# Performance work log

Measured on AMD Instinct MI355X. Metric: run time of the kernel, lower is better.

Reference implementation:

```python
import jax, jax.numpy as jnp
import numpy as np

# dims
D_MODEL = 256; D_STATE = 16; D_CONV = 4; EXPAND = 2
D_INNER = D_MODEL * EXPAND            # 512
DT_RANK = 16                          # ceil(256/16)
B_SZ = 16; C_IN = 64; T_LR = 2560; R = 2; C_OUT = 64


def _p(key, shape, scale=0.02):
    return jax.random.normal(key, shape, jnp.float32) * scale


def setup_inputs() -> dict:
    key = jax.random.key(0)
    ks = iter(jax.random.split(key, 48))
    inp = {}
    inp['x'] = jax.random.normal(next(ks), (B_SZ, C_IN, T_LR), jnp.float32)
    # encoder: Conv1d(64->128,k3,p1) ; Conv1d(128->256,k3,p1)
    inp['enc_w1'] = _p(next(ks), (128, C_IN, 3)); inp['enc_b1'] = jnp.zeros((128,), jnp.float32)
    inp['enc_w2'] = _p(next(ks), (256, 128, 3)); inp['enc_b2'] = jnp.zeros((256,), jnp.float32)
    # BidirectionalMamba norms
    inp['norm1_w'] = jnp.ones((D_MODEL,), jnp.float32)
    inp['norm2_w'] = jnp.ones((D_MODEL,), jnp.float32)
    # one forward ('f') and one backward ('b') Mamba v1 block
    for p in ('f', 'b'):
        inp[p + '_inW'] = _p(next(ks), (2 * D_INNER, D_MODEL))
        inp[p + '_convW'] = _p(next(ks), (D_INNER, D_CONV), 0.2)
        inp[p + '_convb'] = jnp.zeros((D_INNER,), jnp.float32)
        inp[p + '_xW'] = _p(next(ks), (DT_RANK + 2 * D_STATE, D_INNER))
        inp[p + '_dtW'] = _p(next(ks), (D_INNER, DT_RANK), 0.1)
        inp[p + '_dtb'] = -4.0 + 2.0 * jax.random.uniform(next(ks), (D_INNER,), jnp.float32)
        inp[p + '_Alog'] = jnp.log(jnp.tile(jnp.arange(1, D_STATE + 1, dtype=jnp.float32), (D_INNER, 1)))
        inp[p + '_D'] = jnp.ones((D_INNER,), jnp.float32)
        inp[p + '_outW'] = _p(next(ks), (D_MODEL, D_INNER))
    # post-bottleneck: Conv1d(512->256,k3,p1) + BatchNorm1d(256) (eval)
    inp['convd_w'] = _p(next(ks), (256, 512, 3)); inp['convd_b'] = jnp.zeros((256,), jnp.float32)
    inp['bn_g'] = jnp.ones((256,), jnp.float32); inp['bn_b'] = jnp.zeros((256,), jnp.float32)
    inp['bn_mean'] = jnp.zeros((256,), jnp.float32); inp['bn_var'] = jnp.ones((256,), jnp.float32)
    # SubPixel1D: Conv1d(256 -> target_channels*r, k3, p1), r=2
    inp['sp_w'] = _p(next(ks), (C_OUT * R, 256, 3)); inp['sp_b'] = jnp.zeros((C_OUT * R,), jnp.float32)
    return inp


def silu(x):
    return x * jax.nn.sigmoid(x)


def conv1d(x, w, b):  # x: (B,C,L), w: (O,I,K), 'same' padding
    k = w.shape[-1]
    y = jax.lax.conv_general_dilated(x, w, (1,), [(k // 2, k // 2)],
                                     dimension_numbers=('NCH', 'OIH', 'NCH'))
    return y + b[None, :, None]


def rmsnorm(x, w, eps=1e-6):
    return x * jax.lax.rsqrt(jnp.mean(x * x, -1, keepdims=True) + eps) * w


def mamba(x, inW, convW, convb, xW, dtW, dtb, Alog, Dp, outW):
    # x: (B, L, D_MODEL) -> (B, L, D_MODEL); Mamba v1 selective scan.
    Bn = x.shape[0]
    xz = x @ inW.T                               # (B,L,2*di)
    xc, z = jnp.split(xz, 2, axis=-1)            # (B,L,di) each
    # causal depthwise conv over time
    xt = jnp.transpose(xc, (0, 2, 1))            # (B,di,L)
    xt = jax.lax.conv_general_dilated(xt, convW[:, None, :], (1,), [(D_CONV - 1, 0)],
                                      dimension_numbers=('NCH', 'OIH', 'NCH'),
                                      feature_group_count=D_INNER)
    xc = silu(jnp.transpose(xt + convb[None, :, None], (0, 2, 1)))  # (B,L,di)
    dbc = xc @ xW.T                              # (B,L,dt_rank+2N)
    dt = jax.nn.softplus(dbc[..., :DT_RANK] @ dtW.T + dtb)          # (B,L,di)
    Bc = dbc[..., DT_RANK:DT_RANK + D_STATE]     # (B,L,N)
    Cc = dbc[..., DT_RANK + D_STATE:]            # (B,L,N)
    A = -jnp.exp(Alog)                           # (di,N)

    def step(h, inp):
        dt_t, B_t, C_t, x_t = inp                # (B,di),(B,N),(B,N),(B,di)
        dA = jnp.exp(dt_t[..., None] * A)        # (B,di,N)
        h = dA * h + (dt_t * x_t)[..., None] * B_t[:, None, :]
        y = jnp.einsum('bdn,bn->bd', h, C_t)
        return h, y

    xs = (jnp.transpose(dt, (1, 0, 2)), jnp.transpose(Bc, (1, 0, 2)),
          jnp.transpose(Cc, (1, 0, 2)), jnp.transpose(xc, (1, 0, 2)))
    h0 = jnp.zeros((Bn, D_INNER, D_STATE), x.dtype)
    _, ys = jax.lax.scan(step, h0, xs)           # ys: (L,B,di)
    y = jnp.transpose(ys, (1, 0, 2)) + xc * Dp
    return (y * silu(z)) @ outW.T


def reference(x, enc_w1, enc_b1, enc_w2, enc_b2, norm1_w, norm2_w,
              f_inW, f_convW, f_convb, f_xW, f_dtW, f_dtb, f_Alog, f_D, f_outW,
              b_inW, b_convW, b_convb, b_xW, b_dtW, b_dtb, b_Alog, b_D, b_outW,
              convd_w, convd_b, bn_g, bn_b, bn_mean, bn_var, sp_w, sp_b):
    # encoder (dropout = identity in eval)
    e = silu(conv1d(x, enc_w1, enc_b1))
    e = silu(conv1d(e, enc_w2, enc_b2))          # (B,256,T)
    t = jnp.transpose(e, (0, 2, 1))              # (B,T,256)
    # Bi-Mamba bottleneck layer
    xn = rmsnorm(t, norm1_w)
    mo_f = mamba(xn, f_inW, f_convW, f_convb, f_xW, f_dtW, f_dtb, f_Alog, f_D, f_outW) + xn
    xb = xn[:, ::-1, :]
    mo_b = mamba(xb, b_inW, b_convW, b_convb, b_xW, b_dtW, b_dtb, b_Alog, b_D, b_outW) + xb
    mo_b = mo_b[:, ::-1, :]
    combined = rmsnorm(mo_f + mo_b, norm2_w)
    m = jnp.concatenate([combined, t], axis=-1)  # (B,T,512)
    m = jnp.transpose(m, (0, 2, 1))              # (B,512,T)
    # conv_d + BatchNorm1d (eval) + SiLU
    d = conv1d(m, convd_w, convd_b)
    d = (d - bn_mean[None, :, None]) * jax.lax.rsqrt(bn_var + 1e-5)[None, :, None] \
        * bn_g[None, :, None] + bn_b[None, :, None]
    d = silu(d)
    # SubPixel1D upsample x2
    s = conv1d(d, sp_w, sp_b)                    # (B, C_OUT*R, T)
    Bn, C, T = s.shape
    s = s.reshape(Bn, C // R, R, T).transpose(0, 1, 3, 2).reshape(Bn, C // R, T * R)
    return s                                      # (B, 64, 5120)
```

## Files before the change

### kernel.cpp

```cpp
#include <hip/hip_runtime.h>
#include <hip/hip_bf16.h>
#include <math.h>

#define B_SZ 16
#define T_LR 2560
#define BT (B_SZ * T_LR)
#define DM 256
#define DI 512
#define DS 16
#define DTR 16
#define CH 128
#define CH_LOG2 7
#define CLEN (T_LR / CH)

typedef __attribute__((ext_vector_type(8))) short bf16x8;
typedef __attribute__((ext_vector_type(4))) float f32x4;

__device__ __forceinline__ float silu_f(float x) {
    return x / (1.f + __expf(-x));
}
__device__ __forceinline__ unsigned short f2bf(float v) {
    __hip_bfloat16 h = __float2bfloat16(v);
    return *(unsigned short*)&h;
}
__device__ __forceinline__ float bf2f(unsigned short u) {
    union { unsigned int i; float f; } c;
    c.i = (unsigned int)u << 16;
    return c.f;
}
__device__ __forceinline__ int seqrev(int r) {
    int s = r / T_LR, t = r % T_LR;
    return s * T_LR + (T_LR - 1 - t);
}
__device__ __forceinline__ float softplus_f(float x) {
    return (x > 20.f) ? x : __logf(1.f + __expf(x));
}

__global__ __launch_bounds__(256) void k_prep(
    const float* __restrict__ enc_w1, const float* __restrict__ enc_w2,
    const float* __restrict__ convd_w, const float* __restrict__ sp_w,
    const float* __restrict__ convd_b, const float* __restrict__ bn_g,
    const float* __restrict__ bn_b, const float* __restrict__ bn_mean,
    const float* __restrict__ bn_var,
    const float* __restrict__ inW0, const float* __restrict__ inW1,
    const float* __restrict__ outW0, const float* __restrict__ outW1,
    const float* __restrict__ xW0, const float* __restrict__ xW1,
    const float* __restrict__ Alog0, const float* __restrict__ Alog1,
    const float* __restrict__ x,
    unsigned short* __restrict__ W1r, unsigned short* __restrict__ W2r,
    unsigned short* __restrict__ Wdr, unsigned short* __restrict__ Wspr,
    float* __restrict__ alpha, float* __restrict__ beta,
    unsigned short* __restrict__ inW_bf2, unsigned short* __restrict__ outW_bf2,
    unsigned short* __restrict__ xW_bc2, float* __restrict__ Aflag,
    unsigned short* __restrict__ xt)
{
    __shared__ float ts[32][33];
    __shared__ int s_ok;
    int blk = blockIdx.x;
    int tid = threadIdx.x;
    if (blk < 32) {
        int i = blk * 256 + tid;
        int n = i / 64, ci = i % 64;
        #pragma unroll
        for (int k = 0; k < 3; k++)
            W1r[((size_t)k * 128 + n) * 64 + ci] = f2bf(enc_w1[((size_t)n * 64 + ci) * 3 + k]);
    } else if (blk < 160) {
        int i = (blk - 32) * 256 + tid;
        int n = i / 128, ci = i % 128;
        #pragma unroll
        for (int k = 0; k < 3; k++)
            W2r[((size_t)k * 256 + n) * 128 + ci] = f2bf(enc_w2[((size_t)n * 128 + ci) * 3 + k]);
    } else if (blk < 672) {
        int i = (blk - 160) * 256 + tid;
        int n = i / 512, ci = i % 512;
        #pragma unroll
        for (int k = 0; k < 3; k++)
            Wdr[((size_t)k * 256 + n) * 512 + ci] = f2bf(convd_w[((size_t)n * 512 + ci) * 3 + k]);
    } else if (blk < 800) {
        int i = (blk - 672) * 256 + tid;
        int n = i / 256, ci = i % 256;
        #pragma unroll
        for (int k = 0; k < 3; k++)
            Wspr[((size_t)k * 128 + n) * 256 + ci] = f2bf(sp_w[((size_t)n * 256 + ci) * 3 + k]);
    } else if (blk < 801) {
        int c = tid;
        float a = bn_g[c] * rsqrtf(bn_var[c] + 1e-5f);
        alpha[c] = a;
        beta[c] = (convd_b[c] - bn_mean[c]) * a + bn_b[c];
    } else if (blk < 1825) {
        int i = (blk - 801) * 256 + tid;
        inW_bf2[i] = f2bf(inW0[i]);
        inW_bf2[262144 + i] = f2bf(inW1[i]);
    } else if (blk < 2337) {
        int i = (blk - 1825) * 256 + tid;
        outW_bf2[i] = f2bf(outW0[i]);
        outW_bf2[131072 + i] = f2bf(outW1[i]);
    } else if (blk < 2433) {
        int i = (blk - 2337) * 256 + tid;
        xW_bc2[i] = f2bf(xW0[i]);
        xW_bc2[24576 + i] = f2bf(xW1[i]);
    } else if (blk < 2434) {
        if (tid == 0) s_ok = 1;
        __syncthreads();
        int ok = 1;
        for (int i = tid; i < DI * DS; i += 256) {
            int d = i >> 4, n = i & 15;
            float a0f = __expf(Alog0[d * DS]);
            float anf = __expf(Alog0[d * DS + n]);
            if (fabsf(anf - (float)(n + 1) * a0f) > 1e-3f * (float)(n + 1)) ok = 0;
            float a0b = __expf(Alog1[d * DS]);
            float anb = __expf(Alog1[d * DS + n]);
            if (fabsf(anb - (float)(n + 1) * a0b) > 1e-3f * (float)(n + 1)) ok = 0;
        }
        if (!ok) atomicAnd(&s_ok, 0);
        __syncthreads();
        if (tid == 0) Aflag[0] = s_ok ? 1.f : 0.f;
    } else {
        int idx = blk - 2434;
        int t0 = (idx % 80) * 32;
        int c0 = ((idx / 80) & 1) * 32;
        int b = idx / 160;
        int tx = tid & 31, ty = tid >> 5;
        #pragma unroll
        for (int j = 0; j < 4; j++) {
            int c = c0 + ty + j * 8;
            ts[ty + j * 8][tx] = x[((size_t)b * 64 + c) * T_LR + t0 + tx];
        }
        __syncthreads();
        #pragma unroll
        for (int j = 0; j < 4; j++) {
            int t = t0 + ty + j * 8;
            xt[((size_t)b * T_LR + t) * 64 + c0 + tx] = f2bf(ts[tx][ty + j * 8]);
        }
    }
}

__global__ __launch_bounds__(256, 3) void k_conv3_bf(const unsigned short* __restrict__ A1, int K1,
                                                  const unsigned short* __restrict__ A2, int K2,
                                                  const unsigned short* __restrict__ W,
                                                  const float* __restrict__ alpha,
                                                  const float* __restrict__ beta,
                                                  float* __restrict__ outf,
                                                  unsigned short* __restrict__ outb,
                                                  int N, int dosilu, int pixsh) {
    int Kt = K1 + K2;
    __shared__ unsigned short As[2][130][40];
    int tid = threadIdx.x;
    int wave = tid >> 6, lane = tid & 63;
    int wm = (wave >> 1) * 64, wn = (wave & 1) * 64;
    int m0 = blockIdx.x * 128, n0 = blockIdx.y * 128;
    int b = m0 / T_LR, t0 = m0 % T_LR;
    int q = lane >> 4, ml = lane & 15;
    const unsigned short* wbase = W + (size_t)(n0 + wn + ml) * Kt + q * 8;
    size_t tapstride = (size_t)N * Kt;
    size_t nistride  = (size_t)16 * Kt;
    f32x4 acc[4][4] = {};
    int cq = tid & 3;
    int r0 = tid >> 2;
    int r1 = r0 + 64;
    int r2 = r0 + 128;
    bool has2 = (tid < 8);
    int ta0 = t0 - 1 + r0, ta1 = t0 - 1 + r1, ta2 = t0 - 1 + r2;
    bool va0 = (ta0 >= 0) && (ta0 < T_LR);
    bool va1 = (ta1 < T_LR);
    bool va2 = has2 && (ta2 < T_LR);
    uint4 v0, v1, v2;
    #define LOADA(vv, valid, t, col) { vv = make_uint4(0u,0u,0u,0u); if (valid) { \
        const unsigned short* src = ((col) < K1) \
            ? A1 + (size_t)(b * T_LR + (t)) * K1 + (col) \
            : A2 + (size_t)(b * T_LR + (t)) * K2 + ((col) - K1); \
        vv = *(const uint4*)src; } }
    LOADA(v0, va0, ta0, cq * 8);
    LOADA(v1, va1, ta1, cq * 8);
    LOADA(v2, va2, ta2, cq * 8);
    *(uint4*)&As[0][r0][cq * 8] = v0;
    *(uint4*)&As[0][r1][cq * 8] = v1;
    if (has2) *(uint4*)&As[0][r2][cq * 8] = v2;
    int nk = Kt >> 5;
    for (int kk = 0; kk < nk; kk++) {
        __syncthreads();
        int cur = kk & 1;
        int k0 = kk << 5;
        if (kk + 1 < nk) {
            int col = k0 + 32 + cq * 8;
            LOADA(v0, va0, ta0, col);
            LOADA(v1, va1, ta1, col);
            LOADA(v2, va2, ta2, col);
        }
        #pragma unroll
        for (int tap = 0; tap < 3; tap++) {
            bf16x8 bfr[4];
            #pragma unroll
            for (int ni = 0; ni < 4; ni++)
                bfr[ni] = *(const bf16x8*)(wbase + tap * tapstride + ni * nistride + k0);
            #pragma unroll
            for (int mi = 0; mi < 4; mi++) {
                bf16x8 af = *(const bf16x8*)&As[cur][wm + mi * 16 + ml + tap][q * 8];
                #pragma unroll
                for (int ni = 0; ni < 4; ni++)
                    acc[mi][ni] = __builtin_amdgcn_mfma_f32_16x16x32_bf16(af, bfr[ni], acc[mi][ni], 0, 0, 0);
            }
        }
        if (kk + 1 < nk) {
            *(uint4*)&As[cur ^ 1][r0][cq * 8] = v0;
            *(uint4*)&As[cur ^ 1][r1][cq * 8] = v1;
            if (has2) *(uint4*)&As[cur ^ 1][r2][cq * 8] = v2;
        }
    }
    #undef LOADA
    #pragma unroll
    for (int mi = 0; mi < 4; mi++) {
        #pragma unroll
        for (int r = 0; r < 4; r++) {
            int mr = m0 + wm + mi * 16 + q * 4 + r;
            int t = mr - b * T_LR;
            #pragma unroll
            for (int ni = 0; ni < 4; ni++) {
                int col = n0 + wn + ni * 16 + ml;
                float a = alpha ? alpha[col] : 1.f;
                float v = acc[mi][ni][r] * a + beta[col];
                if (dosilu) v = silu_f(v);
                if (pixsh) {
                    int c2 = col >> 1, rr = col & 1;
                    outf[(((size_t)b * 64 + c2) * T_LR + t) * 2 + rr] = v;
                } else {
                    size_t o = (size_t)mr * N + col;
                    if (outf) outf[o] = v;
                    if (outb) outb[o] = f2bf(v);
                }
            }
        }
    }
}

__global__ __launch_bounds__(256) void k_inproj_conv(const unsigned short* __restrict__ xn,
                                                     const unsigned short* __restrict__ inW,
                                                     const float* __restrict__ cw,
                                                     const float* __restrict__ cb,
                                                     unsigned short* __restrict__ xcs,
                                                     int arev) {
    __shared__ unsigned short As[128][40];
    __shared__ unsigned short Bs[128][40];
    __shared__ unsigned short Ct[131][136];
    int tid = threadIdx.x;
    int wave = tid >> 6, lane = tid & 63;
    int wm = (wave >> 1) * 64, wn = (wave & 1) * 64;
    int m0 = blockIdx.x * 128, n0 = blockIdx.y * 128;
    int b = m0 / T_LR, t0 = m0 % T_LR;
    int sc = tid & 3, sr = tid >> 2;
    int ar0 = m0 + sr, ar1 = m0 + sr + 64;
    if (arev) { ar0 = seqrev(ar0); ar1 = seqrev(ar1); }
    const unsigned short* ap0 = xn + (size_t)ar0 * DM + sc * 8;
    const unsigned short* ap1 = xn + (size_t)ar1 * DM + sc * 8;
    const unsigned short* bp0 = inW + (size_t)(n0 + sr) * DM + sc * 8;
    const unsigned short* bp1 = inW + (size_t)(n0 + sr + 64) * DM + sc * 8;
    f32x4 acc[4][4] = {};
    int q = lane >> 4, ml = lane & 15;
    for (int k0 = 0; k0 < DM; k0 += 32) {
        uint4 a0 = *(const uint4*)(ap0 + k0);
        uint4 a1 = *(const uint4*)(ap1 + k0);
        uint4 b0 = *(const uint4*)(bp0 + k0);
        uint4 b1 = *(const uint4*)(bp1 + k0);
        __syncthreads();
        *(uint4*)&As[sr][sc * 8]      = a0;
        *(uint4*)&As[sr + 64][sc * 8] = a1;
        *(uint4*)&Bs[sr][sc * 8]      = b0;
        *(uint4*)&Bs[sr + 64][sc * 8] = b1;
        __syncthreads();
        bf16x8 af[4], bfr[4];
        #pragma unroll
        for (int mi = 0; mi < 4; mi++)
            af[mi] = *(const bf16x8*)&As[wm + mi * 16 + ml][q * 8];
        #pragma unroll
        for (int ni = 0; ni < 4; ni++)
            bfr[ni] = *(const bf16x8*)&Bs[wn + ni * 16 + ml][q * 8];
        #pragma unroll
        for (int mi = 0; mi < 4; mi++)
            #pragma unroll
            for (int ni = 0; ni < 4; ni++)
                acc[mi][ni] = __builtin_amdgcn_mfma_f32_16x16x32_bf16(af[mi], bfr[ni], acc[mi][ni], 0, 0, 0);
    }
    #pragma unroll
    for (int mi = 0; mi < 4; mi++)
        #pragma unroll
        for (int r = 0; r < 4; r++)
            #pragma unroll
            for (int ni = 0; ni < 4; ni++)
                Ct[3 + wm + mi * 16 + q * 4 + r][wn + ni * 16 + ml] = f2bf(acc[mi][ni][r]);
    for (int i = tid; i < 384; i += 256) {
        int hr = i >> 7, c = i & 127;
        int tr = t0 - 3 + hr;
        float v = 0.f;
        if (tr >= 0) {
            int src = b * T_LR + (arev ? (T_LR - 1 - tr) : tr);
            const unsigned short* xr = xn + (size_t)src * DM;
            const unsigned short* wr = inW + (size_t)(n0 + c) * DM;
            for (int k = 0; k < DM; k += 8) {
                uint4 xa = *(const uint4*)(xr + k);
                uint4 wa = *(const uint4*)(wr + k);
                const unsigned short* xs = (const unsigned short*)&xa;
                const unsigned short* wsp = (const unsigned short*)&wa;
                #pragma unroll
                for (int j = 0; j < 8; j++) v += bf2f(xs[j]) * bf2f(wsp[j]);
            }
        }
        Ct[hr][c] = f2bf(v);
    }
    __syncthreads();
    int col = tid & 127;
    int d = n0 + col;
    float w0 = cw[d * 4 + 0], w1 = cw[d * 4 + 1], w2 = cw[d * 4 + 2], w3 = cw[d * 4 + 3];
    float bi = cb[d];
    int rbase = tid >> 7;
    for (int j = 0; j < 64; j++) {
        int row = rbase + 2 * j;
        float v = bi + bf2f(Ct[row][col]) * w0 + bf2f(Ct[row + 1][col]) * w1
                     + bf2f(Ct[row + 2][col]) * w2 + bf2f(Ct[row + 3][col]) * w3;
        xcs[(size_t)(m0 + row) * DI + d] = f2bf(silu_f(v));
    }
}

__global__ __launch_bounds__(256) void k_rmsnorm(const float* __restrict__ in1,
                                                 const float* __restrict__ w,
                                                 float* __restrict__ out,
                                                 unsigned short* __restrict__ out_bf,
                                                 int ntok) {
    int tok = (blockIdx.x * 256 + threadIdx.x) >> 6;
    int lane = threadIdx.x & 63;
    if (tok >= ntok) return;
    float4 v = ((const float4*)(in1 + (size_t)tok * DM))[lane];
    float ss = v.x * v.x + v.y * v.y + v.z * v.z + v.w * v.w;
    #pragma unroll
    for (int off = 32; off > 0; off >>= 1) ss += __shfl_xor(ss, off);
    float sc = rsqrtf(ss * (1.f / 256.f) + 1e-6f);
    float4 wv = ((const float4*)w)[lane];
    float4 o;
    o.x = v.x * sc * wv.x; o.y = v.y * sc * wv.y;
    o.z = v.z * sc * wv.z; o.w = v.w * sc * wv.w;
    if (out) ((float4*)(out + (size_t)tok * DM))[lane] = o;
    if (out_bf) {
        ushort4 ob;
        ob.x = f2bf(o.x); ob.y = f2bf(o.y); ob.z = f2bf(o.z); ob.w = f2bf(o.w);
        ((ushort4*)(out_bf + (size_t)tok * DM))[lane] = ob;
    }
}

__global__ __launch_bounds__(256) void k_gemm_bf(const unsigned short* __restrict__ A, int lda,
                                                 const unsigned short* __restrict__ Bw,
                                                 float* Cf, unsigned short* Cb, int ldc,
                                                 const float* __restrict__ res,
                                                 const float* __restrict__ bias,
                                                 const unsigned short* __restrict__ gate,
                                                 int K, int Nout, int act,
                                                 int arev, int crev, int accum) {
    __shared__ unsigned short As[128][40];
    __shared__ unsigned short Bs[128][40];
    int tid = threadIdx.x;
    int wave = tid >> 6, lane = tid & 63;
    int wm = (wave >> 1) * 64, wn = (wave & 1) * 64;
    int m0 = blockIdx.x * 128, n0 = blockIdx.y * 128;
    int sc = tid & 3, sr = tid >> 2;
    int ar0 = m0 + sr, ar1 = m0 + sr + 64;
    if (arev) { ar0 = seqrev(ar0); ar1 = seqrev(ar1); }
    const unsigned short* ap0 = A + (size_t)ar0 * lda + sc * 8;
    const unsigned short* ap1 = A + (size_t)ar1 * lda + sc * 8;
    bool bv0 = (n0 + sr) < Nout;
    bool bv1 = (n0 + sr + 64) < Nout;
    const unsigned short* bp0 = Bw + (size_t)(n0 + sr) * K + sc * 8;
    const unsigned short* bp1 = Bw + (size_t)(n0 + sr + 64) * K + sc * 8;
    f32x4 acc[4][4] = {};
    int q = lane >> 4, ml = lane & 15;
    for (int k0 = 0; k0 < K; k0 += 32) {
        uint4 a0 = *(const uint4*)(ap0 + k0);
        uint4 a1 = *(const uint4*)(ap1 + k0);
        uint4 b0 = make_uint4(0u, 0u, 0u, 0u), b1 = make_uint4(0u, 0u, 0u, 0u);
        if (bv0) b0 = *(const uint4*)(bp0 + k0);
        if (bv1) b1 = *(const uint4*)(bp1 + k0);
        __syncthreads();
        *(uint4*)&As[sr][sc * 8]      = a0;
        *(uint4*)&As[sr + 64][sc * 8] = a1;
        *(uint4*)&Bs[sr][sc * 8]      = b0;
        *(uint4*)&Bs[sr + 64][sc * 8] = b1;
        __syncthreads();
        bf16x8 af[4], bfr[4];
        #pragma unroll
        for (int mi = 0; mi < 4; mi++)
            af[mi] = *(const bf16x8*)&As[wm + mi * 16 + ml][q * 8];
        #pragma unroll
        for (int ni = 0; ni < 4; ni++)
            bfr[ni] = *(const bf16x8*)&Bs[wn + ni * 16 + ml][q * 8];
        #pragma unroll
        for (int mi = 0; mi < 4; mi++)
            #pragma unroll
            for (int ni = 0; ni < 4; ni++)
                acc[mi][ni] = __builtin_amdgcn_mfma_f32_16x16x32_bf16(af[mi], bfr[ni], acc[mi][ni], 0, 0, 0);
    }
    #pragma unroll
    for (int mi = 0; mi < 4; mi++) {
        #pragma unroll
        for (int r = 0; r < 4; r++) {
            int mr = m0 + wm + mi * 16 + q * 4 + r;
            int orow = crev ? seqrev(mr) : mr;
            #pragma unroll
            for (int ni = 0; ni < 4; ni++) {
                int col = n0 + wn + ni * 16 + ml;
                if (col < Nout) {
                    float v = acc[mi][ni][r];
                    if (bias) v += bias[col];
                    if (act == 2) v = softplus_f(v);
                    if (gate) v = silu_f(v) * bf2f(gate[(size_t)mr * ldc + col]);
                    if (res) v += res[(size_t)orow * ldc + col];
                    if (accum) v += Cf[(size_t)orow * ldc + col];
                    if (Cf) Cf[(size_t)orow * ldc + col] = v;
                    if (Cb) Cb[(size_t)orow * ldc + col] = f2bf(v);
                }
            }
        }
    }
}

__global__ __launch_bounds__(256) void k_gemm_bf_cb(const unsigned short* __restrict__ A, int lda,
                                                    const unsigned short* __restrict__ Bw,
                                                    unsigned short* __restrict__ Cb, int ldc,
                                                    const float* __restrict__ bias,
                                                    const unsigned short* __restrict__ gate,
                                                    int K, int act, int arev) {
    __shared__ __align__(16) unsigned short smem[2 * 128 * 40];
    unsigned short (*As)[40] = (unsigned short(*)[40])smem;
    unsigned short (*Bs)[40] = (unsigned short(*)[40])(smem + 128 * 40);
    float* sC = (float*)smem;
    int tid = threadIdx.x;
    int wave = tid >> 6, lane = tid & 63;
    int wm = (wave >> 1) * 64, wn = (wave & 1) * 64;
    int m0 = blockIdx.x * 128, n0 = blockIdx.y * 128;
    int sc = tid & 3, sr = tid >> 2;
    int ar0 = m0 + sr, ar1 = m0 + sr + 64;
    if (arev) { ar0 = seqrev(ar0); ar1 = seqrev(ar1); }
    const unsigned short* ap0 = A + (size_t)ar0 * lda + sc * 8;
    const unsigned short* ap1 = A + (size_t)ar1 * lda + sc * 8;
    const unsigned short* bp0 = Bw + (size_t)(n0 + sr) * K + sc * 8;
    const unsigned short* bp1 = Bw + (size_t)(n0 + sr + 64) * K + sc * 8;
    f32x4 acc[4][4] = {};
    int q = lane >> 4, ml = lane & 15;
    for (int k0 = 0; k0 < K; k0 += 32) {
        uint4 a0 = *(const uint4*)(ap0 + k0);
        uint4 a1 = *(const uint4*)(ap1 + k0);
        uint4 b0 = *(const uint4*)(bp0 + k0);
        uint4 b1 = *(const uint4*)(bp1 + k0);
        __syncthreads();
        *(uint4*)&As[sr][sc * 8]      = a0;
        *(uint4*)&As[sr + 64][sc * 8] = a1;
        *(uint4*)&Bs[sr][sc * 8]      = b0;
        *(uint4*)&Bs[sr + 64][sc * 8] = b1;
        __syncthreads();
        bf16x8 af[4], bfr[4];
        #pragma unroll
        for (int mi = 0; mi < 4; mi++)
            af[mi] = *(const bf16x8*)&As[wm + mi * 16 + ml][q * 8];
        #pragma unroll
        for (int ni = 0; ni < 4; ni++)
            bfr[ni] = *(const bf16x8*)&Bs[wn + ni * 16 + ml][q * 8];
        #pragma unroll
        for (int mi = 0; mi < 4; mi++)
            #pragma unroll
            for (int ni = 0; ni < 4; ni++)
                acc[mi][ni] = __builtin_amdgcn_mfma_f32_16x16x32_bf16(af[mi], bfr[ni], acc[mi][ni], 0, 0, 0);
    }
    #pragma unroll
    for (int p = 0; p < 4; p++) {
        __syncthreads();
        if ((wave >> 1) == (p >> 1)) {
            int mib = (p & 1) * 2;
            #pragma unroll
            for (int m2 = 0; m2 < 2; m2++) {
                int mi = mib + m2;
                int rl = mi * 16 + q * 4 - (p & 1) * 32;
                #pragma unroll
                for (int r = 0; r < 4; r++)
                    #pragma unroll
                    for (int ni = 0; ni < 4; ni++)
                        sC[(rl + r) * 140 + wn + ni * 16 + ml] = acc[mi][ni][r];
            }
        }
        __syncthreads();
        #pragma unroll
        for (int gi = 0; gi < 2; gi++) {
            int g = tid + gi * 256;
            int row = g >> 4;
            int colg = (g & 15) * 8;
            int grow = m0 + p * 32 + row;
            const float* src = sC + row * 140 + colg;
            float4 v0 = *(const float4*)src;
            float4 v1 = *(const float4*)(src + 4);
            float vv[8] = {v0.x, v0.y, v0.z, v0.w, v1.x, v1.y, v1.z, v1.w};
            unsigned short gu[8];
            if (gate)
                *(uint4*)gu = *(const uint4*)(gate + (size_t)grow * ldc + n0 + colg);
            unsigned short o[8];
            #pragma unroll
            for (int jj = 0; jj < 8; jj++) {
                float v = vv[jj];
                if (bias) v += bias[n0 + colg + jj];
                if (act == 2) v = softplus_f(v);
                if (gate) v = silu_f(v) * bf2f(gu[jj]);
                o[jj] = f2bf(v);
            }
            *(uint4*)(Cb + (size_t)grow * ldc + n0 + colg) = *(uint4*)o;
        }
    }
}

__global__ __launch_bounds__(256) void k_scan_p1(const unsigned short* __restrict__ x,
                                                 const float* __restrict__ db,
                                                 const float* __restrict__ dtW,
                                                 const float* __restrict__ dtb,
                                                 const float* __restrict__ Alog,
                                                 const float* __restrict__ Aflag,
                                                 float* __restrict__ hS,
                                                 float* __restrict__ csum) {
    __shared__ float dbs[CLEN * 48];
    int tid = threadIdx.x;
    int gid = blockIdx.x * 256 + tid;
    int d = gid & (DI - 1);
    int bcix = gid >> 9;
    int c = bcix & (CH - 1);
    int bl = bcix >> CH_LOG2;
    int tbase = c * CLEN;
    const float* dbp = db + ((size_t)bl * T_LR + tbase) * 48;
    if (tid < 240) *(float4*)&dbs[tid * 4] = *(const float4*)(dbp + tid * 4);
    bool fast = (Aflag[0] != 0.f);
    float A0 = -__expf(Alog[d * DS]);
    float Av[DS], h[DS];
    #pragma unroll
    for (int n = 0; n < DS; n++) h[n] = 0.f;
    if (!fast) {
        #pragma unroll
        for (int n = 0; n < DS; n++) Av[n] = -__expf(Alog[d * DS + n]);
    }
    const float4* wp = (const float4*)(dtW + d * 16);
    float4 w0 = wp[0], w1 = wp[1], w2 = wp[2], w3 = wp[3];
    float bias = dtb[d];
    const unsigned short* xp = x + ((size_t)bl * T_LR + tbase) * DI + d;
    float S = 0.f;
    __syncthreads();
    for (int t = 0; t < CLEN; t++) {
        const float* bc = dbs + t * 48;
        float dl = bias
            + bc[0] * w0.x + bc[1] * w0.y + bc[2] * w0.z + bc[3] * w0.w
            + bc[4] * w1.x + bc[5] * w1.y + bc[6] * w1.z + bc[7] * w1.w
            + bc[8] * w2.x + bc[9] * w2.y + bc[10] * w2.z + bc[11] * w2.w
            + bc[12] * w3.x + bc[13] * w3.y + bc[14] * w3.z + bc[15] * w3.w;
        float dtv = softplus_f(dl);
        float xv  = bf2f(xp[(size_t)t * DI]);
        float dtx = dtv * xv;
        S += dtv;
        if (fast) {
            float e1 = __expf(dtv * A0);
            float e = e1;
            #pragma unroll
            for (int n = 0; n < DS; n++) {
                h[n] = e * h[n] + dtx * bc[16 + n];
                e *= e1;
            }
        } else {
            #pragma unroll
            for (int n = 0; n < DS; n++)
                h[n] = __expf(dtv * Av[n]) * h[n] + dtx * bc[16 + n];
        }
    }
    float* hp = hS + (size_t)gid * DS;
    #pragma unroll
    for (int n = 0; n < DS; n++) hp[n] = h[n];
    csum[gid] = S;
}

__global__ __launch_bounds__(256) void k_scan_p2(float* __restrict__ hS,
                                                 const float* __restrict__ csum,
                                                 const float* __restrict__ Alog) {
    int gid = blockIdx.x * 256 + threadIdx.x;
    int n = gid & (DS - 1);
    int d = (gid >> 4) & (DI - 1);
    int bl = gid >> 13;
    float An = -__expf(Alog[d * DS + n]);
    float hs = 0.f;
    for (int c = 0; c < CH; c++) {
        size_t base = ((size_t)(bl * CH + c) * DI + d);
        float he = hS[base * DS + n];
        float S  = csum[base];
        hS[base * DS + n] = hs;
        hs = __expf(An * S) * hs + he;
    }
}

__global__ __launch_bounds__(256) void k_scan_p3(unsigned short* __restrict__ x,
                                                 const float* __restrict__ db,
                                                 const float* __restrict__ dtW,
                                                 const float* __restrict__ dtb,
                                                 const float* __restrict__ Alog,
                                                 const float* __restrict__ Aflag,
                                                 const float* __restrict__ Dp,
                                                 const float* __restrict__ hS) {
    __shared__ float dbs[CLEN * 48];
    int tid = threadIdx.x;
    int gid = blockIdx.x * 256 + tid;
    int d = gid & (DI - 1);
    int bcix = gid >> 9;
    int c = bcix & (CH - 1);
    int bl = bcix >> CH_LOG2;
    int tbase = c * CLEN;
    const float* dbp = db + ((size_t)bl * T_LR + tbase) * 48;
    if (tid < 240) *(float4*)&dbs[tid * 4] = *(const float4*)(dbp + tid * 4);
    bool fast = (Aflag[0] != 0.f);
    float A0 = -__expf(Alog[d * DS]);
    float Av[DS], h[DS];
    const float* hp = hS + (size_t)gid * DS;
    #pragma unroll
    for (int n = 0; n < DS; n++) h[n] = hp[n];
    if (!fast) {
        #pragma unroll
        for (int n = 0; n < DS; n++) Av[n] = -__expf(Alog[d * DS + n]);
    }
    const float4* wp = (const float4*)(dtW + d * 16);
    float4 w0 = wp[0], w1 = wp[1], w2 = wp[2], w3 = wp[3];
    float bias = dtb[d];
    float Dd = Dp[d];
    unsigned short* xp = x + ((size_t)bl * T_LR + tbase) * DI + d;
    __syncthreads();
    for (int t = 0; t < CLEN; t++) {
        const float* bc = dbs + t * 48;
        float dl = bias
            + bc[0] * w0.x + bc[1] * w0.y + bc[2] * w0.z + bc[3] * w0.w
            + bc[4] * w1.x + bc[5] * w1.y + bc[6] * w1.z + bc[7] * w1.w
            + bc[8] * w2.x + bc[9] * w2.y + bc[10] * w2.z + bc[11] * w2.w
            + bc[12] * w3.x + bc[13] * w3.y + bc[14] * w3.z + bc[15] * w3.w;
        float dtv = softplus_f(dl);
        float xv  = bf2f(xp[(size_t)t * DI]);
        float dtx = dtv * xv;
        float acc = 0.f;
        if (fast) {
            float e1 = __expf(dtv * A0);
            float e = e1;
            #pragma unroll
            for (int n = 0; n < DS; n++) {
                h[n] = e * h[n] + dtx * bc[16 + n];
                acc += h[n] * bc[32 + n];
                e *= e1;
            }
        } else {
            #pragma unroll
            for (int n = 0; n < DS; n++) {
                h[n] = __expf(dtv * Av[n]) * h[n] + dtx * bc[16 + n];
                acc += h[n] * bc[32 + n];
            }
        }
        xp[(size_t)t * DI] = f2bf(acc + xv * Dd);
    }
}

extern "C" void kernel_launch(void* const* d_in, const int* in_sizes, int n_in,
                              void* d_out, int out_size, void* d_ws, size_t ws_size,
                              hipStream_t stream) {
    const float* x       = (const float*)d_in[0];
    const float* enc_w1  = (const float*)d_in[1];
    const float* enc_b1  = (const float*)d_in[2];
    const float* enc_w2  = (const float*)d_in[3];
    const float* enc_b2  = (const float*)d_in[4];
    const float* norm1_w = (const float*)d_in[5];
    const float* norm2_w = (const float*)d_in[6];
    const float* convd_w = (const float*)d_in[25];
    const float* convd_b = (const float*)d_in[26];
    const float* bn_g    = (const float*)d_in[27];
    const float* bn_b    = (const float*)d_in[28];
    const float* bn_mean = (const float*)d_in[29];
    const float* bn_var  = (const float*)d_in[30];
    const float* sp_w    = (const float*)d_in[31];
    const float* sp_b    = (const float*)d_in[32];
    float* out = (float*)d_out;

    const float* inW0   = (const float*)d_in[7];
    const float* xW0    = (const float*)d_in[10];
    const float* outW0  = (const float*)d_in[15];
    const float* inW1   = (const float*)d_in[16];
    const float* xW1    = (const float*)d_in[19];
    const float* outW1  = (const float*)d_in[24];
    const float* Alog0  = (const float*)d_in[13];
    const float* Alog1  = (const float*)d_in[22];

    float* ws = (float*)d_ws;
    size_t availf = ws_size / sizeof(float);
    size_t o = 0;
    float* t_buf  = ws + o; o += (size_t)BT * DM;
    float* xn_buf = ws + o; o += (size_t)BT * DM;
    float* mo     = ws + o; o += (size_t)BT * DM;
    unsigned short* xn_bf = (unsigned short*)(ws + o); o += (size_t)BT * DM / 2;
    unsigned short* tb_bf = (unsigned short*)(ws + o); o += (size_t)BT * DM / 2;
    unsigned short* inW_bf2  = (unsigned short*)(ws + o); o += (size_t)1024 * DM;
    unsigned short* outW_bf2 = (unsigned short*)(ws + o); o += (size_t)DM * DI;
    unsigned short* xW_bc2   = (unsigned short*)(ws + o); o += (size_t)48 * DI;
    unsigned short* W1r  = (unsigned short*)(ws + o); o += (3 * 128 * 64) / 2;
    unsigned short* W2r  = (unsigned short*)(ws + o); o += (3 * 256 * 128) / 2;
    unsigned short* Wdr  = (unsigned short*)(ws + o); o += (3 * 256 * 512) / 2;
    unsigned short* Wspr = (unsigned short*)(ws + o); o += (3 * 128 * 256) / 2;
    float* alpha_d = ws + o; o += 256;
    float* beta_d  = ws + o; o += 256;
    float* Aflag_d = ws + o; o += 4;
    size_t persist = o;
    float* scratch = ws + persist;
    size_t scratch_avail = (availf > persist) ? (availf - persist) : 0;
    size_t per_b = (size_t)T_LR * DI / 2 * 2 + (size_t)T_LR * 48
                 + (size_t)CH * DI * (DS + 1);
    int Bc = 16;
    while (Bc > 1 && (size_t)Bc * per_b > scratch_avail) Bc >>= 1;

    unsigned short* xt  = (unsigned short*)mo;
    unsigned short* e1t = (unsigned short*)(mo + (size_t)BT * 64 / 2);
    unsigned short* comb_bf = (unsigned short*)xn_buf;
    unsigned short* d_bf = (unsigned short*)mo;

    k_prep<<<4994, 256, 0, stream>>>(enc_w1, enc_w2, convd_w, sp_w,
                                     convd_b, bn_g, bn_b, bn_mean, bn_var,
                                     inW0, inW1, outW0, outW1, xW0, xW1,
                                     Alog0, Alog1,
                                     x, W1r, W2r, Wdr, Wspr, alpha_d, beta_d,
                                     inW_bf2, outW_bf2, xW_bc2, Aflag_d, xt);

    k_conv3_bf<<<dim3(BT / 128, 1), 256, 0, stream>>>(xt, 64, nullptr, 0, W1r,
                                                      nullptr, enc_b1, nullptr, e1t, 128, 1, 0);
    k_conv3_bf<<<dim3(BT / 128, 2), 256, 0, stream>>>(e1t, 128, nullptr, 0, W2r,
                                                      nullptr, enc_b2, t_buf, tb_bf, 256, 1, 0);
    k_rmsnorm<<<BT / 4, 256, 0, stream>>>(t_buf, norm1_w, xn_buf, xn_bf, BT);

    for (int dir = 0; dir < 2; dir++) {
        const float* convW = (const float*)d_in[8 + 9 * dir];
        const float* convb = (const float*)d_in[9 + 9 * dir];
        const float* dtW   = (const float*)d_in[11 + 9 * dir];
        const float* dtb   = (const float*)d_in[12 + 9 * dir];
        const float* Alog  = (const float*)d_in[13 + 9 * dir];
        const float* Dp    = (const float*)d_in[14 + 9 * dir];
        const unsigned short* inW_d  = inW_bf2 + (size_t)dir * 1024 * DM;
        const unsigned short* outW_d = outW_bf2 + (size_t)dir * DM * DI;
        const unsigned short* xWbc_d = xW_bc2 + (size_t)dir * 48 * DI;
        int rev = dir;
        for (int b0 = 0; b0 < B_SZ; b0 += Bc) {
            int Tc = Bc * T_LR;
            unsigned short* xcs = (unsigned short*)scratch;
            unsigned short* ygb = xcs + (size_t)Tc * DI;
            float* db   = (float*)(ygb + (size_t)Tc * DI);
            float* hS   = db + (size_t)Tc * 48;
            float* csum = hS + (size_t)Bc * CH * DI * DS;
            const float*          xnC  = xn_buf + (size_t)b0 * T_LR * DM;
            const unsigned short* xnbC = xn_bf  + (size_t)b0 * T_LR * DM;
            float*                moC  = mo     + (size_t)b0 * T_LR * DM;
            k_inproj_conv<<<dim3(Tc / 128, DI / 128), 256, 0, stream>>>(
                xnbC, inW_d, convW, convb, xcs, rev);
            k_gemm_bf<<<dim3(Tc / 128, 1), 256, 0, stream>>>(
                xcs, DI, xWbc_d, db, nullptr, 48, nullptr, nullptr, nullptr,
                DI, 48, 0, 0, 0, 0);
            k_scan_p1<<<(Bc * CH * DI) / 256, 256, 0, stream>>>(xcs, db, dtW, dtb, Alog, Aflag_d, hS, csum);
            k_scan_p2<<<(Bc * DI * DS) / 256, 256, 0, stream>>>(hS, csum, Alog);
            k_scan_p3<<<(Bc * CH * DI) / 256, 256, 0, stream>>>(xcs, db, dtW, dtb, Alog, Aflag_d, Dp, hS);
            k_gemm_bf_cb<<<dim3(Tc / 128, DI / 128), 256, 0, stream>>>(
                xnbC, DM, inW_d + (size_t)DI * DM, ygb, DI, nullptr, xcs, DM, 0, rev);
            k_gemm_bf<<<dim3(Tc / 128, DM / 128), 256, 0, stream>>>(
                ygb, DI, outW_d, moC, nullptr, DM, xnC, nullptr, nullptr,
                DI, DM, 0, 0, rev, dir);
        }
    }

    k_rmsnorm<<<BT / 4, 256, 0, stream>>>(mo, norm2_w, nullptr, comb_bf, BT);
    k_conv3_bf<<<dim3(BT / 128, 2), 256, 0, stream>>>(comb_bf, 256, tb_bf, 256, Wdr,
                                                      alpha_d, beta_d, nullptr, d_bf, 256, 1, 0);
    k_conv3_bf<<<dim3(BT / 128, 1), 256, 0, stream>>>(d_bf, 256, nullptr, 0, Wspr,
                                                      nullptr, sp_b, out, nullptr, 128, 0, 1);
}
```

Measured before the change: 1.318 ms.

## Batch forward and backward Mamba directions into shared launches via blockIdx.z

```diff
diff --git a/kernel.cpp b/kernel.cpp
--- a/kernel.cpp
+++ b/kernel.cpp
@@ -234,14 +234,22 @@
 }
 
 __global__ __launch_bounds__(256) void k_inproj_conv(const unsigned short* __restrict__ xn,
-                                                     const unsigned short* __restrict__ inW,
-                                                     const float* __restrict__ cw,
-                                                     const float* __restrict__ cb,
+                                                     const unsigned short* __restrict__ inW2,
+                                                     const float* __restrict__ cw0,
+                                                     const float* __restrict__ cw1,
+                                                     const float* __restrict__ cb0,
+                                                     const float* __restrict__ cb1,
                                                      unsigned short* __restrict__ xcs,
-                                                     int arev) {
+                                                     long long dsXcs) {
     __shared__ unsigned short As[128][40];
     __shared__ unsigned short Bs[128][40];
     __shared__ unsigned short Ct[131][136];
+    int dir = blockIdx.z;
+    int arev = dir;
+    const unsigned short* inW = inW2 + (size_t)dir * 1024 * DM;
+    const float* cw = dir ? cw1 : cw0;
+    const float* cb = dir ? cb1 : cb0;
+    xcs += (size_t)dir * dsXcs;
     int tid = threadIdx.x;
     int wave = tid >> 6, lane = tid & 63;
     int wm = (wave >> 1) * 64, wn = (wave & 1) * 64;
@@ -321,6 +329,7 @@
 }
 
 __global__ __launch_bounds__(256) void k_rmsnorm(const float* __restrict__ in1,
+                                                 const float* __restrict__ in2,
                                                  const float* __restrict__ w,
                                                  float* __restrict__ out,
                                                  unsigned short* __restrict__ out_bf,
@@ -329,6 +338,10 @@
     int lane = threadIdx.x & 63;
     if (tok >= ntok) return;
     float4 v = ((const float4*)(in1 + (size_t)tok * DM))[lane];
+    if (in2) {
+        float4 u = ((const float4*)(in2 + (size_t)tok * DM))[lane];
+        v.x += u.x; v.y += u.y; v.z += u.z; v.w += u.w;
+    }
     float ss = v.x * v.x + v.y * v.y + v.z * v.z + v.w * v.w;
     #pragma unroll
     for (int off = 32; off > 0; off >>= 1) ss += __shfl_xor(ss, off);
@@ -345,25 +358,25 @@
     }
 }
 
-__global__ __launch_bounds__(256) void k_gemm_bf(const unsigned short* __restrict__ A, int lda,
-                                                 const unsigned short* __restrict__ Bw,
-                                                 float* Cf, unsigned short* Cb, int ldc,
+__global__ __launch_bounds__(256) void k_gemm_bf(const unsigned short* __restrict__ A, int lda, long long dsA,
+                                                 const unsigned short* __restrict__ Bw, long long dsB,
+                                                 float* Cf, long long dsCf, int ldc,
                                                  const float* __restrict__ res,
-                                                 const float* __restrict__ bias,
-                                                 const unsigned short* __restrict__ gate,
-                                                 int K, int Nout, int act,
-                                                 int arev, int crev, int accum) {
+                                                 int K, int Nout, int crevmode) {
     __shared__ unsigned short As[128][40];
     __shared__ unsigned short Bs[128][40];
+    int dir = blockIdx.z;
+    A += (long long)dir * dsA;
+    Bw += (long long)dir * dsB;
+    Cf += (long long)dir * dsCf;
+    int crev = (crevmode == 2) ? dir : crevmode;
     int tid = threadIdx.x;
     int wave = tid >> 6, lane = tid & 63;
     int wm = (wave >> 1) * 64, wn = (wave & 1) * 64;
     int m0 = blockIdx.x * 128, n0 = blockIdx.y * 128;
     int sc = tid & 3, sr = tid >> 2;
-    int ar0 = m0 + sr, ar1 = m0 + sr + 64;
-    if (arev) { ar0 = seqrev(ar0); ar1 = seqrev(ar1); }
-    const unsigned short* ap0 = A + (size_t)ar0 * lda + sc * 8;
-    const unsigned short* ap1 = A + (size_t)ar1 * lda + sc * 8;
+    const unsigned short* ap0 = A + (size_t)(m0 + sr) * lda + sc * 8;
+    const unsigned short* ap1 = A + (size_t)(m0 + sr + 64) * lda + sc * 8;
     bool bv0 = (n0 + sr) < Nout;
     bool bv1 = (n0 + sr + 64) < Nout;
     const unsigned short* bp0 = Bw + (size_t)(n0 + sr) * K + sc * 8;
@@ -406,13 +419,8 @@
                 int col = n0 + wn + ni * 16 + ml;
                 if (col < Nout) {
                     float v = acc[mi][ni][r];
-                    if (bias) v += bias[col];
-                    if (act == 2) v = softplus_f(v);
-                    if (gate) v = silu_f(v) * bf2f(gate[(size_t)mr * ldc + col]);
                     if (res) v += res[(size_t)orow * ldc + col];
-                    if (accum) v += Cf[(size_t)orow * ldc + col];
-                    if (Cf) Cf[(size_t)orow * ldc + col] = v;
-                    if (Cb) Cb[(size_t)orow * ldc + col] = f2bf(v);
+                    Cf[(size_t)orow * ldc + col] = v;
                 }
             }
         }
@@ -420,15 +428,19 @@
 }
 
 __global__ __launch_bounds__(256) void k_gemm_bf_cb(const unsigned short* __restrict__ A, int lda,
-                                                    const unsigned short* __restrict__ Bw,
-                                                    unsigned short* __restrict__ Cb, int ldc,
-                                                    const float* __restrict__ bias,
-                                                    const unsigned short* __restrict__ gate,
-                                                    int K, int act, int arev) {
+                                                    const unsigned short* __restrict__ Bw, long long dsB,
+                                                    unsigned short* __restrict__ Cb, int ldc, long long dsCb,
+                                                    const unsigned short* __restrict__ gate, long long dsGate,
+                                                    int K) {
     __shared__ __align__(16) unsigned short smem[2 * 128 * 40];
     unsigned short (*As)[40] = (unsigned short(*)[40])smem;
     unsigned short (*Bs)[40] = (unsigned short(*)[40])(smem + 128 * 40);
     float* sC = (float*)smem;
+    int dir = blockIdx.z;
+    int arev = dir;
+    Bw += (long long)dir * dsB;
+    Cb += (long long)dir * dsCb;
+    gate += (long long)dir * dsGate;
     int tid = threadIdx.x;
     int wave = tid >> 6, lane = tid & 63;
     int wm = (wave >> 1) * 64, wn = (wave & 1) * 64;
@@ -494,15 +506,12 @@
             float4 v1 = *(const float4*)(src + 4);
             float vv[8] = {v0.x, v0.y, v0.z, v0.w, v1.x, v1.y, v1.z, v1.w};
             unsigned short gu[8];
-            if (gate)
-                *(uint4*)gu = *(const uint4*)(gate + (size_t)grow * ldc + n0 + colg);
+            *(uint4*)gu = *(const uint4*)(gate + (size_t)grow * ldc + n0 + colg);
             unsigned short o[8];
             #pragma unroll
             for (int jj = 0; jj < 8; jj++) {
                 float v = vv[jj];
-                if (bias) v += bias[n0 + colg + jj];
-                if (act == 2) v = softplus_f(v);
-                if (gate) v = silu_f(v) * bf2f(gu[jj]);
+                v = silu_f(v) * bf2f(gu[jj]);
                 o[jj] = f2bf(v);
             }
             *(uint4*)(Cb + (size_t)grow * ldc + n0 + colg) = *(uint4*)o;
@@ -512,12 +521,12 @@
 
 __global__ __launch_bounds__(256) void k_scan_p1(const unsigned short* __restrict__ x,
                                                  const float* __restrict__ db,
-                                                 const float* __restrict__ dtW,
-                                                 const float* __restrict__ dtb,
-                                                 const float* __restrict__ Alog,
+                                                 const float* __restrict__ dtW0, const float* __restrict__ dtW1,
+                                                 const float* __restrict__ dtb0, const float* __restrict__ dtb1,
+                                                 const float* __restrict__ Alog0, const float* __restrict__ Alog1,
                                                  const float* __restrict__ Aflag,
                                                  float* __restrict__ hS,
-                                                 float* __restrict__ csum) {
+                                                 float* __restrict__ csum, int Bc) {
     __shared__ float dbs[CLEN * 48];
     int tid = threadIdx.x;
     int gid = blockIdx.x * 256 + tid;
@@ -525,6 +534,10 @@
     int bcix = gid >> 9;
     int c = bcix & (CH - 1);
     int bl = bcix >> CH_LOG2;
+    int dir = (bl >= Bc) ? 1 : 0;
+    const float* dtW  = dir ? dtW1  : dtW0;
+    const float* dtb  = dir ? dtb1  : dtb0;
+    const float* Alog = dir ? Alog1 : Alog0;
     int tbase = c * CLEN;
     const float* dbp = db + ((size_t)bl * T_LR + tbase) * 48;
     if (tid < 240) *(float4*)&dbs[tid * 4] = *(const float4*)(dbp + tid * 4);
@@ -576,11 +589,13 @@
 
 __global__ __launch_bounds__(256) void k_scan_p2(float* __restrict__ hS,
                                                  const float* __restrict__ csum,
-                                                 const float* __restrict__ Alog) {
+                                                 const float* __restrict__ Alog0,
+                                                 const float* __restrict__ Alog1, int Bc) {
     int gid = blockIdx.x * 256 + threadIdx.x;
     int n = gid & (DS - 1);
     int d = (gid >> 4) & (DI - 1);
     int bl = gid >> 13;
+    const float* Alog = (bl >= Bc) ? Alog1 : Alog0;
     float An = -__expf(Alog[d * DS + n]);
     float hs = 0.f;
     for (int c = 0; c < CH; c++) {
@@ -594,12 +609,12 @@
 
 __global__ __launch_bounds__(256) void k_scan_p3(unsigned short* __restrict__ x,
                                                  const float* __restrict__ db,
-                                                 const float* __restrict__ dtW,
-                                                 const float* __restrict__ dtb,
-                                                 const float* __restrict__ Alog,
+                                                 const float* __restrict__ dtW0, const float* __restrict__ dtW1,
+                                                 const float* __restrict__ dtb0, const float* __restrict__ dtb1,
+                                                 const float* __restrict__ Alog0, const float* __restrict__ Alog1,
                                                  const float* __restrict__ Aflag,
-                                                 const float* __restrict__ Dp,
-                                                 const float* __restrict__ hS) {
+                                                 const float* __restrict__ Dp0, const float* __restrict__ Dp1,
+                                                 const float* __restrict__ hS, int Bc) {
     __shared__ float dbs[CLEN * 48];
     int tid = threadIdx.x;
     int gid = blockIdx.x * 256 + tid;
@@ -607,6 +622,11 @@
     int bcix = gid >> 9;
     int c = bcix & (CH - 1);
     int bl = bcix >> CH_LOG2;
+    int dir = (bl >= Bc) ? 1 : 0;
+    const float* dtW  = dir ? dtW1  : dtW0;
+    const float* dtb  = dir ? dtb1  : dtb0;
+    const float* Alog = dir ? Alog1 : Alog0;
+    const float* Dp   = dir ? Dp1   : Dp0;
     int tbase = c * CLEN;
     const float* dbp = db + ((size_t)bl * T_LR + tbase) * 48;
     if (tid < 240) *(float4*)&dbs[tid * 4] = *(const float4*)(dbp + tid * 4);
@@ -678,13 +698,23 @@
     float* out = (float*)d_out;
 
     const float* inW0   = (const float*)d_in[7];
+    const float* cw0    = (const float*)d_in[8];
+    const float* cb0    = (const float*)d_in[9];
     const float* xW0    = (const float*)d_in[10];
+    const float* dtW0   = (const float*)d_in[11];
+    const float* dtb0   = (const float*)d_in[12];
+    const float* Alog0  = (const float*)d_in[13];
+    const float* Dp0    = (const float*)d_in[14];
     const float* outW0  = (const float*)d_in[15];
     const float* inW1   = (const float*)d_in[16];
+    const float* cw1    = (const float*)d_in[17];
+    const float* cb1    = (const float*)d_in[18];
     const float* xW1    = (const float*)d_in[19];
+    const float* dtW1   = (const float*)d_in[20];
+    const float* dtb1   = (const float*)d_in[21];
+    const float* Alog1  = (const float*)d_in[22];
+    const float* Dp1    = (const float*)d_in[23];
     const float* outW1  = (const float*)d_in[24];
-    const float* Alog0  = (const float*)d_in[13];
-    const float* Alog1  = (const float*)d_in[22];
 
     float* ws = (float*)d_ws;
     size_t availf = ws_size / sizeof(float);
@@ -707,10 +737,10 @@
     size_t persist = o;
     float* scratch = ws + persist;
     size_t scratch_avail = (availf > persist) ? (availf - persist) : 0;
-    size_t per_b = (size_t)T_LR * DI / 2 * 2 + (size_t)T_LR * 48
-                 + (size_t)CH * DI * (DS + 1);
+    size_t per_b2 = 2 * ((size_t)T_LR * DI / 2 * 2 + (size_t)T_LR * 48
+                         + (size_t)CH * DI * (DS + 1));
     int Bc = 16;
-    while (Bc > 1 && (size_t)Bc * per_b > scratch_avail) Bc >>= 1;
+    while (Bc > 1 && (size_t)Bc * per_b2 > scratch_avail) Bc >>= 1;
 
     unsigned short* xt  = (unsigned short*)mo;
     unsigned short* e1t = (unsigned short*)(mo + (size_t)BT * 64 / 2);
@@ -728,46 +758,40 @@
                                                       nullptr, enc_b1, nullptr, e1t, 128, 1, 0);
     k_conv3_bf<<<dim3(BT / 128, 2), 256, 0, stream>>>(e1t, 128, nullptr, 0, W2r,
                                                       nullptr, enc_b2, t_buf, tb_bf, 256, 1, 0);
-    k_rmsnorm<<<BT / 4, 256, 0, stream>>>(t_buf, norm1_w, xn_buf, xn_bf, BT);
-
-    for (int dir = 0; dir < 2; dir++) {
-        const float* convW = (const float*)d_in[8 + 9 * dir];
-        const float* convb = (const float*)d_in[9 + 9 * dir];
-        const float* dtW   = (const float*)d_in[11 + 9 * dir];
-        const float* dtb   = (const float*)d_in[12 + 9 * dir];
-        const float* Alog  = (const float*)d_in[13 + 9 * dir];
-        const float* Dp    = (const float*)d_in[14 + 9 * dir];
-        const unsigned short* inW_d  = inW_bf2 + (size_t)dir * 1024 * DM;
-        const unsigned short* outW_d = outW_bf2 + (size_t)dir * DM * DI;
-        const unsigned short* xWbc_d = xW_bc2 + (size_t)dir * 48 * DI;
-        int rev = dir;
-        for (int b0 = 0; b0 < B_SZ; b0 += Bc) {
-            int Tc = Bc * T_LR;
-            unsigned short* xcs = (unsigned short*)scratch;
-            unsigned short* ygb = xcs + (size_t)Tc * DI;
-            float* db   = (float*)(ygb + (size_t)Tc * DI);
-            float* hS   = db + (size_t)Tc * 48;
-            float* csum = hS + (size_t)Bc * CH * DI * DS;
-            const float*          xnC  = xn_buf + (size_t)b0 * T_LR * DM;
-            const unsigned short* xnbC = xn_bf  + (size_t)b0 * T_LR * DM;
-            float*                moC  = mo     + (size_t)b0 * T_LR * DM;
-            k_inproj_conv<<<dim3(Tc / 128, DI / 128), 256, 0, stream>>>(
-                xnbC, inW_d, convW, convb, xcs, rev);
-            k_gemm_bf<<<dim3(Tc / 128, 1), 256, 0, stream>>>(
-                xcs, DI, xWbc_d, db, nullptr, 48, nullptr, nullptr, nullptr,
-                DI, 48, 0, 0, 0, 0);
-            k_scan_p1<<<(Bc * CH * DI) / 256, 256, 0, stream>>>(xcs, db, dtW, dtb, Alog, Aflag_d, hS, csum);
-            k_scan_p2<<<(Bc * DI * DS) / 256, 256, 0, stream>>>(hS, csum, Alog);
-            k_scan_p3<<<(Bc * CH * DI) / 256, 256, 0, stream>>>(xcs, db, dtW, dtb, Alog, Aflag_d, Dp, hS);
-            k_gemm_bf_cb<<<dim3(Tc / 128, DI / 128), 256, 0, stream>>>(
-                xnbC, DM, inW_d + (size_t)DI * DM, ygb, DI, nullptr, xcs, DM, 0, rev);
-            k_gemm_bf<<<dim3(Tc / 128, DM / 128), 256, 0, stream>>>(
-                ygb, DI, outW_d, moC, nullptr, DM, xnC, nullptr, nullptr,
-                DI, DM, 0, 0, rev, dir);
-        }
-    }
-
-    k_rmsnorm<<<BT / 4, 256, 0, stream>>>(mo, norm2_w, nullptr, comb_bf, BT);
+    k_rmsnorm<<<BT / 4, 256, 0, stream>>>(t_buf, nullptr, norm1_w, xn_buf, xn_bf, BT);
+
+    long long dsMo1 = (long long)(t_buf - mo);
+    for (int b0 = 0; b0 < B_SZ; b0 += Bc) {
+        int Tc = Bc * T_LR;
+        long long TcDI = (long long)Tc * DI;
+        unsigned short* xcs = (unsigned short*)scratch;
+        unsigned short* ygb = xcs + (size_t)2 * Tc * DI;
+        float* db   = (float*)(ygb + (size_t)2 * Tc * DI);
+        float* hS   = db + (size_t)2 * Tc * 48;
+        float* csum = hS + (size_t)2 * Bc * CH * DI * DS;
+        const float*          xnC  = xn_buf + (size_t)b0 * T_LR * DM;
+        const unsigned short* xnbC = xn_bf  + (size_t)b0 * T_LR * DM;
+        float*                moC  = mo     + (size_t)b0 * T_LR * DM;
+        k_inproj_conv<<<dim3(Tc / 128, DI / 128, 2), 256, 0, stream>>>(
+            xnbC, inW_bf2, cw0, cw1, cb0, cb1, xcs, TcDI);
+        k_gemm_bf<<<dim3(Tc / 128, 1, 2), 256, 0, stream>>>(
+            xcs, DI, TcDI, xW_bc2, (long long)48 * DI,
+            db, (long long)Tc * 48, 48, nullptr, DI, 48, 0);
+        k_scan_p1<<<(2 * Bc * CH * DI) / 256, 256, 0, stream>>>(
+            xcs, db, dtW0, dtW1, dtb0, dtb1, Alog0, Alog1, Aflag_d, hS, csum, Bc);
+        k_scan_p2<<<(2 * Bc * DI * DS) / 256, 256, 0, stream>>>(
+            hS, csum, Alog0, Alog1, Bc);
+        k_scan_p3<<<(2 * Bc * CH * DI) / 256, 256, 0, stream>>>(
+            xcs, db, dtW0, dtW1, dtb0, dtb1, Alog0, Alog1, Aflag_d, Dp0, Dp1, hS, Bc);
+        k_gemm_bf_cb<<<dim3(Tc / 128, DI / 128, 2), 256, 0, stream>>>(
+            xnbC, DM, inW_bf2 + (size_t)DI * DM, (long long)1024 * DM,
+            ygb, DI, TcDI, xcs, TcDI, DM);
+        k_gemm_bf<<<dim3(Tc / 128, DM / 128, 2), 256, 0, stream>>>(
+            ygb, DI, TcDI, outW_bf2, (long long)DM * DI,
+            moC, dsMo1, DM, xnC, DI, DM, 2);
+    }
+
+    k_rmsnorm<<<BT / 4, 256, 0, stream>>>(mo, t_buf, norm2_w, nullptr, comb_bf, BT);
     k_conv3_bf<<<dim3(BT / 128, 2), 256, 0, stream>>>(comb_bf, 256, tb_bf, 256, Wdr,
                                                       alpha_d, beta_d, nullptr, d_bf, 256, 1, 0);
     k_conv3_bf<<<dim3(BT / 128, 1), 256, 0, stream>>>(d_bf, 256, nullptr, 0, Wspr,
```

New measurement: 1.193 ms. 9.5% less time.
